# Optimization experiments

Measured on AMD Instinct MI355X. Metric: run time of the kernel, lower is better.

## Reference

```python
import jax, jax.numpy as jnp
import numpy as np

D_MODEL = 1024
NUM_HEADS = 16
HEAD_DIM = D_MODEL // NUM_HEADS
B, S = 2, 2048


def setup_inputs() -> dict:
    key = jax.random.key(0)
    ks = jax.random.split(key, 8)
    scale = 1.0 / np.sqrt(D_MODEL)
    inp = {
        "query": jax.random.normal(ks[0], (B, S, D_MODEL), jnp.float32),
        "key": jax.random.normal(ks[1], (B, S, D_MODEL), jnp.float32),
        "value": jax.random.normal(ks[2], (B, S, D_MODEL), jnp.float32),
        # causal mask, broadcastable over batch and heads
        "mask": jnp.tril(jnp.ones((S, S), dtype=bool))[None, None, :, :],
        # torch nn.Linear weights: y = x @ W.T (+ b)
        "Wq": jax.random.normal(ks[3], (D_MODEL, D_MODEL), jnp.float32) * scale,
        "Wk": jax.random.normal(ks[4], (D_MODEL, D_MODEL), jnp.float32) * scale,
        "Wv": jax.random.normal(ks[5], (D_MODEL, D_MODEL), jnp.float32) * scale,
        "Wo": jax.random.normal(ks[6], (D_MODEL, D_MODEL), jnp.float32) * scale,
        "bo": jax.random.normal(ks[7], (D_MODEL,), jnp.float32) * scale,
    }
    return inp


def _split_heads(x):
    b, s, _ = x.shape
    return x.reshape(b, s, NUM_HEADS, HEAD_DIM).transpose(0, 2, 1, 3)  # [B,H,S,Dh]


def reference(query, key, value, mask, Wq, Wk, Wv, Wo, bo):
    q = _split_heads(query @ Wq.T)
    k = _split_heads(key @ Wk.T)
    v = _split_heads(value @ Wv.T)
    scores = jnp.einsum("bhqd,bhkd->bhqk", q, k) / jnp.sqrt(jnp.float32(HEAD_DIM))
    scores = jnp.where(mask, scores, jnp.float32(-jnp.inf))
    attn = jax.nn.softmax(scores, axis=-1)
    out = jnp.einsum("bhqk,bhkd->bhqd", attn, v)  # [B,H,S,Dh]
    out = out.transpose(0, 2, 1, 3).reshape(query.shape[0], q.shape[2], D_MODEL)
    return out @ Wo.T + bo
```

## Files before the change

### kernel.cpp

```cpp
#include <hip/hip_runtime.h>
#include <hip/hip_bf16.h>

#define DM   1024
#define NH   16
#define HD   64
#define SEQ  2048
#define BATCH 2
#define MTOT (BATCH*SEQ)

typedef unsigned short u16;
typedef __attribute__((ext_vector_type(8))) short bf16x8;
typedef __attribute__((ext_vector_type(4))) float f32x4;

#define SC2F 0.1803368801111464f

__device__ __forceinline__ float bf2f(u16 h) {
  union { unsigned int i; float f; } u; u.i = ((unsigned int)h) << 16; return u.f;
}
__device__ __forceinline__ u16 f2bf(float f) {
  union { float f; unsigned int i; } u; u.f = f;
  unsigned int r = u.i + 0x7fffu + ((u.i >> 16) & 1u);
  return (u16)(r >> 16);
}
__device__ __forceinline__ unsigned int pk2(float lo, float hi) {
  union { float f; unsigned int u; } a, b; a.f = lo; b.f = hi;
  return ((a.u + 0x8000u) >> 16) | ((b.u + 0x8000u) & 0xFFFF0000u);
}
__device__ __forceinline__ unsigned int cvtpk(float lo, float hi) {
  unsigned int r;
  asm("v_cvt_pk_bf16_f32 %0, %1, %2" : "=v"(r) : "v"(lo), "v"(hi));
  return r;
}

__device__ __forceinline__ uint4 load8_bf16(const void* base, size_t elemOff, bool isf32) {
  if (!isf32) return *(const uint4*)((const u16*)base + elemOff);
  const float* f = (const float*)base + elemOff;
  f32x4 a = *(const f32x4*)f;
  f32x4 b = *(const f32x4*)(f + 4);
  union { u16 h[8]; uint4 v; } r;
  r.h[0]=f2bf(a[0]); r.h[1]=f2bf(a[1]); r.h[2]=f2bf(a[2]); r.h[3]=f2bf(a[3]);
  r.h[4]=f2bf(b[0]); r.h[5]=f2bf(b[1]); r.h[6]=f2bf(b[2]); r.h[7]=f2bf(b[3]);
  return r.v;
}

__global__ __launch_bounds__(256) void prep(
    const void* __restrict__ q, const void* __restrict__ k, const void* __restrict__ v,
    const void* __restrict__ wq, const void* __restrict__ wk, const void* __restrict__ wv,
    const void* __restrict__ wo, const void* __restrict__ bo,
    u16* __restrict__ Xq, u16* __restrict__ Xk, u16* __restrict__ Xv,
    u16* __restrict__ Wqb, u16* __restrict__ Wkb, u16* __restrict__ Wvb, u16* __restrict__ Wob,
    float* __restrict__ biasf, int* __restrict__ flag_out)
{
  const int tid = threadIdx.x;
  __shared__ int cnts[4];
  {
    const u16* qs = (const u16*)q;
    int e0 = (qs[tid*2]   >> 7) & 0xFF;
    int e1 = (qs[tid*2+1] >> 7) & 0xFF;
    int c = ((e0 >= 0x6E && e0 <= 0x8F) ? 1 : 0) + ((e1 >= 0x6E && e1 <= 0x8F) ? 1 : 0);
    c += __shfl_xor(c, 1);  c += __shfl_xor(c, 2);  c += __shfl_xor(c, 4);
    c += __shfl_xor(c, 8);  c += __shfl_xor(c, 16); c += __shfl_xor(c, 32);
    if ((tid & 63) == 0) cnts[tid >> 6] = c;
  }
  __syncthreads();
  const bool isf32 = (cnts[0] + cnts[1] + cnts[2] + cnts[3]) < 400;

  const int z = blockIdx.z;
  if (z == 7) {
    if (blockIdx.x == 0) {
      if (tid == 0) *flag_out = isf32 ? 0 : 1;
      for (int i = tid; i < DM; i += 256)
        biasf[i] = isf32 ? ((const float*)bo)[i] : bf2f(((const u16*)bo)[i]);
    }
    return;
  }
  const void* src; u16* dst; size_t n;
  switch (z) {
    case 0: src=q;  dst=Xq;  n=(size_t)MTOT*DM; break;
    case 1: src=k;  dst=Xk;  n=(size_t)MTOT*DM; break;
    case 2: src=v;  dst=Xv;  n=(size_t)MTOT*DM; break;
    case 3: src=wq; dst=Wqb; n=(size_t)DM*DM;   break;
    case 4: src=wk; dst=Wkb; n=(size_t)DM*DM;   break;
    case 5: src=wv; dst=Wvb; n=(size_t)DM*DM;   break;
    default: src=wo; dst=Wob; n=(size_t)DM*DM;  break;
  }
  const size_t stride = (size_t)gridDim.x * 256 * 8;
  for (size_t i = ((size_t)blockIdx.x * 256 + tid) * 8; i < n; i += stride)
    *(uint4*)(dst + i) = load8_bf16(src, i, isf32);
}

__device__ __forceinline__ void gld16(const u16* g, u16* l) {
  __builtin_amdgcn_global_load_lds(
      (const __attribute__((address_space(1))) void*)g,
      (__attribute__((address_space(3))) void*)l, 16, 0, 0);
}

__global__ __launch_bounds__(256) void gemm_qkv(
    const u16* __restrict__ X0, const u16* __restrict__ X1, const u16* __restrict__ X2,
    const u16* __restrict__ W0, const u16* __restrict__ W1, const u16* __restrict__ W2,
    u16* __restrict__ F0, u16* __restrict__ F1, u16* __restrict__ F2)
{
  __shared__ __align__(16) u16 smem[16384];
  u16* const A0 = smem;
  u16* const A1 = smem + 4096;
  u16* const B0 = smem + 8192;
  u16* const B1 = smem + 12288;

  const int zz = blockIdx.z;
  const u16* X = (zz==0) ? X0 : ((zz==1) ? X1 : X2);
  const u16* W = (zz==0) ? W0 : ((zz==1) ? W1 : W2);
  u16* outF    = (zz==0) ? F0 : ((zz==1) ? F1 : F2);

  const int tid = threadIdx.x;
  const int wave = tid >> 6, lane = tid & 63, quad = lane >> 4, l16 = lane & 15;
  const int wr = wave >> 1, wc = wave & 1;
  const int m0 = blockIdx.x * 128, n0 = blockIdx.y * 128;

  const int sg = ((lane & 3) ^ ((lane >> 3) & 3)) * 8;
  const int rS = wave*32 + (lane >> 2);
  const u16* gA0 = X + (size_t)(m0 + rS)*DM + sg;
  const u16* gA1 = X + (size_t)(m0 + rS + 16)*DM + sg;
  const u16* gB0 = W + (size_t)(n0 + rS)*DM + sg;
  const u16* gB1 = W + (size_t)(n0 + rS + 16)*DM + sg;
  const int so = wave*1024;

  const int xslot8 = (quad ^ ((l16 >> 1) & 3)) * 8;

  f32x4 acc[4][4];
#pragma unroll
  for (int i = 0; i < 4; i++)
#pragma unroll
    for (int j = 0; j < 4; j++) { acc[i][j][0]=0.f; acc[i][j][1]=0.f; acc[i][j][2]=0.f; acc[i][j][3]=0.f; }

  gld16(gA0, A0 + so);
  gld16(gA1, A0 + so + 512);
  gld16(gB0, B0 + so);
  gld16(gB1, B0 + so + 512);
  asm volatile("" ::: "memory");

  for (int k0 = 0; k0 < DM; k0 += 32) {
    const int cb = (k0 >> 5) & 1;
    u16* const Ab = cb ? A1 : A0;
    u16* const Bb = cb ? B1 : B0;
    if (k0 + 32 < DM) {
      u16* const An = cb ? A0 : A1;
      u16* const Bn = cb ? B0 : B1;
      gld16(gA0 + k0 + 32, An + so);
      gld16(gA1 + k0 + 32, An + so + 512);
      gld16(gB0 + k0 + 32, Bn + so);
      gld16(gB1 + k0 + 32, Bn + so + 512);
      asm volatile("s_waitcnt vmcnt(4)" ::: "memory");
    } else {
      asm volatile("s_waitcnt vmcnt(0)" ::: "memory");
    }
    __builtin_amdgcn_s_barrier();
    asm volatile("" ::: "memory");

    bf16x8 af[4], bfr[4];
#pragma unroll
    for (int fr = 0; fr < 4; fr++)
      af[fr] = *(const bf16x8*)&Ab[(wr*64 + fr*16 + l16)*32 + xslot8];
#pragma unroll
    for (int fc = 0; fc < 4; fc++)
      bfr[fc] = *(const bf16x8*)&Bb[(wc*64 + fc*16 + l16)*32 + xslot8];
#pragma unroll
    for (int fr = 0; fr < 4; fr++)
#pragma unroll
      for (int fc = 0; fc < 4; fc++)
        acc[fr][fc] = __builtin_amdgcn_mfma_f32_16x16x32_bf16(af[fr], bfr[fc], acc[fr][fc], 0, 0, 0);

    asm volatile("" ::: "memory");
    __builtin_amdgcn_s_barrier();
    asm volatile("" ::: "memory");
  }

  if (zz == 2) {
    u16* const Ts = smem;
    const int bb = m0 >> 11;
    const int s0 = m0 & (SEQ-1);
#pragma unroll
    for (int p = 0; p < 2; p++) {
      __syncthreads();
      if (wc == p) {
#pragma unroll
        for (int fr = 0; fr < 4; fr++) {
#pragma unroll
          for (int fc = 0; fc < 4; fc++) {
            const int dl = fc*16 + l16;
            const int sb = wr*64 + fr*16 + quad*4;
            const int slot = (sb >> 3) ^ (dl & 15);
            u16* rowp = &Ts[dl*128 + slot*8 + (sb & 7)];
            *(unsigned int*)(rowp)     = pk2(acc[fr][fc][0], acc[fr][fc][1]);
            *(unsigned int*)(rowp + 2) = pk2(acc[fr][fc][2], acc[fr][fc][3]);
          }
        }
      }
      __syncthreads();
      const int dl2 = tid >> 2, ch4 = tid & 3;
      const int hh = (n0 + p*64) >> 6;
      u16* dst = outF + ((size_t)(bb*NH + hh)*HD + dl2)*SEQ + s0 + ch4*32;
#pragma unroll
      for (int j = 0; j < 4; j++) {
        const int c  = ch4*4 + j;
        const int lo = (c >> 2)*32 + (c & 3)*4;
        const int hi = lo + 16;
        uint2 lo2 = *(const uint2*)&Ts[dl2*128 + (((lo >> 3) ^ (dl2 & 15))*8) + (lo & 7)];
        uint2 hi2 = *(const uint2*)&Ts[dl2*128 + (((hi >> 3) ^ (dl2 & 15))*8) + (hi & 7)];
        uint4 o; o.x = lo2.x; o.y = lo2.y; o.z = hi2.x; o.w = hi2.y;
        *(uint4*)&dst[j*8] = o;
      }
    }
    return;
  }

#pragma unroll
  for (int fr = 0; fr < 4; fr++) {
#pragma unroll
    for (int rr = 0; rr < 4; rr++) {
      const int m = m0 + wr*64 + fr*16 + quad*4 + rr;
#pragma unroll
      for (int fc = 0; fc < 4; fc++) {
        const int n = n0 + wc*64 + fc*16 + l16;
        float vv = acc[fr][fc][rr];
        if (zz == 0) vv *= SC2F;
        const int b = m >> 11, s = m & (SEQ-1), h = n >> 6, d = n & (HD-1);
        outF[((size_t)(b*NH + h)*SEQ + s)*HD + d] = f2bf(vv);
      }
    }
  }
}

__global__ __launch_bounds__(256) void gemm_out(
    const u16* __restrict__ X, const u16* __restrict__ W,
    const float* __restrict__ biasf, void* __restrict__ outP,
    const int* __restrict__ dflag)
{
  __shared__ __align__(16) u16 smem[12288];
  u16* const A0 = smem;
  u16* const A1 = smem + 4096;
  u16* const B0 = smem + 8192;
  u16* const B1 = smem + 10240;

  const int tid = threadIdx.x;
  const int wave = tid >> 6, lane = tid & 63, quad = lane >> 4, l16 = lane & 15;
  const int wr = wave >> 1, wc = wave & 1;
  const int m0 = blockIdx.x * 128, n0 = blockIdx.y * 64;

  const int sg = ((lane & 3) ^ ((lane >> 3) & 3)) * 8;
  const int rA = wave*32 + (lane >> 2);
  const int rB = wave*16 + (lane >> 2);
  const u16* gA0 = X + (size_t)(m0 + rA)*DM + sg;
  const u16* gA1 = X + (size_t)(m0 + rA + 16)*DM + sg;
  const u16* gB0 = W + (size_t)(n0 + rB)*DM + sg;
  const int soA = wave*1024, soB = wave*512;

  const int xslot8 = (quad ^ ((l16 >> 1) & 3)) * 8;

  f32x4 acc[4][2];
#pragma unroll
  for (int i = 0; i < 4; i++)
#pragma unroll
    for (int j = 0; j < 2; j++) { acc[i][j][0]=0.f; acc[i][j][1]=0.f; acc[i][j][2]=0.f; acc[i][j][3]=0.f; }

  gld16(gA0, A0 + soA);
  gld16(gA1, A0 + soA + 512);
  gld16(gB0, B0 + soB);
  asm volatile("" ::: "memory");

  for (int k0 = 0; k0 < DM; k0 += 32) {
    const int cb = (k0 >> 5) & 1;
    u16* const Ab = cb ? A1 : A0;
    u16* const Bb = cb ? B1 : B0;
    if (k0 + 32 < DM) {
      u16* const An = cb ? A0 : A1;
      u16* const Bn = cb ? B0 : B1;
      gld16(gA0 + k0 + 32, An + soA);
      gld16(gA1 + k0 + 32, An + soA + 512);
      gld16(gB0 + k0 + 32, Bn + soB);
      asm volatile("s_waitcnt vmcnt(3)" ::: "memory");
    } else {
      asm volatile("s_waitcnt vmcnt(0)" ::: "memory");
    }
    __builtin_amdgcn_s_barrier();
    asm volatile("" ::: "memory");

    bf16x8 af[4], bfr[2];
#pragma unroll
    for (int fr = 0; fr < 4; fr++)
      af[fr] = *(const bf16x8*)&Ab[(wr*64 + fr*16 + l16)*32 + xslot8];
#pragma unroll
    for (int fc = 0; fc < 2; fc++)
      bfr[fc] = *(const bf16x8*)&Bb[(wc*32 + fc*16 + l16)*32 + xslot8];
#pragma unroll
    for (int fr = 0; fr < 4; fr++)
#pragma unroll
      for (int fc = 0; fc < 2; fc++)
        acc[fr][fc] = __builtin_amdgcn_mfma_f32_16x16x32_bf16(af[fr], bfr[fc], acc[fr][fc], 0, 0, 0);

    asm volatile("" ::: "memory");
    __builtin_amdgcn_s_barrier();
    asm volatile("" ::: "memory");
  }

  const bool isf32 = (*dflag == 0);
#pragma unroll
  for (int fr = 0; fr < 4; fr++) {
#pragma unroll
    for (int rr = 0; rr < 4; rr++) {
      const int m = m0 + wr*64 + fr*16 + quad*4 + rr;
#pragma unroll
      for (int fc = 0; fc < 2; fc++) {
        const int n = n0 + wc*32 + fc*16 + l16;
        float vv = acc[fr][fc][rr] + biasf[n];
        if (isf32) ((float*)outP)[(size_t)m*DM + n] = vv;
        else       ((u16*)outP)[(size_t)m*DM + n]   = f2bf(vv);
      }
    }
  }
}

__global__ __launch_bounds__(256) void attn_mfma(
    const u16* __restrict__ Qb, const u16* __restrict__ Kb,
    const u16* __restrict__ Vtb,
    u16* __restrict__ Opart, float* __restrict__ mlpart)
{
  __shared__ u16 Ks[2][64*64];
  __shared__ u16 Vs[2][64*64];

  const int bh = blockIdx.x;
  const int pr = blockIdx.y, z = blockIdx.z;
  const u16* Qp = Qb  + (size_t)bh * SEQ * HD;
  const u16* Kp = Kb  + (size_t)bh * SEQ * HD;
  const u16* Vp = Vtb + (size_t)bh * HD * SEQ;

  const int tid  = threadIdx.x;
  const int wave = tid >> 6, lane = tid & 63, quad = lane >> 4, l16 = lane & 15;

  const int i0 = wave*128 + lane, i1 = i0 + 64;
  const int r0 = i0 >> 3, c0 = (i0 & 7) ^ (r0 & 7);
  const int r1 = i1 >> 3, c1 = (i1 & 7) ^ (r1 & 7);
  const int kq_off0 = r0*HD + c0*8;
  const int kq_off1 = r1*HD + c1*8;
  const int v_off0  = r0*SEQ + c0*8;
  const int v_off1  = r1*SEQ + c1*8;

  const int l7 = l16 & 7;
  const int ql = wave*16 + l16;
  const int so = wave*1024;

  for (int ph = 0; ph < 2; ph++) {
    const int qt = ph ? (31 - pr) : pr;
    const int n = qt + 1, half = (n + 1) >> 1;
    const int klo = z ? half : 0, khi = z ? n : half;
    const int q0 = qt * 64;
    const int qg = q0 + ql;

    const u16* qrow = Qp + (size_t)qg * HD;
    const bf16x8 bq0 = *(const bf16x8*)(qrow + quad*8);
    const bf16x8 bq1 = *(const bf16x8*)(qrow + 32 + quad*8);

    f32x4 O[4];
#pragma unroll
    for (int u = 0; u < 4; u++) { O[u][0]=0.f; O[u][1]=0.f; O[u][2]=0.f; O[u][3]=0.f; }
    float mi = -__builtin_inff(), li = 0.f;

    if (klo < khi) {
      gld16(Kp + klo*(64*HD) + kq_off0, &Ks[0][so]);
      gld16(Kp + klo*(64*HD) + kq_off1, &Ks[0][so + 512]);
      gld16(Vp + klo*64 + v_off0, &Vs[0][so]);
      gld16(Vp + klo*64 + v_off1, &Vs[0][so + 512]);
    }
    asm volatile("" ::: "memory");

    for (int kt = klo; kt < khi; kt++) {
      const int cb = (kt - klo) & 1;
      const u16* kb = &Ks[cb][0];
      const u16* vb = &Vs[cb][0];
      if (kt + 1 < khi) {
        u16* kn = &Ks[cb ^ 1][so];
        u16* vn = &Vs[cb ^ 1][so];
        gld16(Kp + (kt+1)*(64*HD) + kq_off0, kn);
        gld16(Kp + (kt+1)*(64*HD) + kq_off1, kn + 512);
        gld16(Vp + (kt+1)*64 + v_off0, vn);
        gld16(Vp + (kt+1)*64 + v_off1, vn + 512);
        asm volatile("s_waitcnt vmcnt(4)" ::: "memory");
      } else {
        asm volatile("s_waitcnt vmcnt(0)" ::: "memory");
      }
      __builtin_amdgcn_s_barrier();
      asm volatile("" ::: "memory");

      f32x4 st[4];
#pragma unroll
      for (int t = 0; t < 4; t++) { st[t][0]=0.f; st[t][1]=0.f; st[t][2]=0.f; st[t][3]=0.f; }
#pragma unroll
      for (int s = 0; s < 2; s++) {
        const bf16x8 bq = s ? bq1 : bq0;
        const int ch = s*4 + quad;
#pragma unroll
        for (int t = 0; t < 4; t++) {
          bf16x8 ak = *(const bf16x8*)&kb[((t*16 + l16)*8 + (ch ^ l7))*8];
          st[t] = __builtin_amdgcn_mfma_f32_16x16x32_bf16(ak, bq, st[t], 0, 0, 0);
        }
      }

      if (kt == qt) {
#pragma unroll
        for (int t = 0; t < 4; t++)
#pragma unroll
          for (int r = 0; r < 4; r++)
            if (kt*64 + t*16 + quad*4 + r > qg) st[t][r] = -__builtin_inff();
      }

      float a0 = fmaxf(fmaxf(st[0][0], st[0][1]), fmaxf(st[0][2], st[0][3]));
      float a1 = fmaxf(fmaxf(st[1][0], st[1][1]), fmaxf(st[1][2], st[1][3]));
      float a2 = fmaxf(fmaxf(st[2][0], st[2][1]), fmaxf(st[2][2], st[2][3]));
      float a3 = fmaxf(fmaxf(st[3][0], st[3][1]), fmaxf(st[3][2], st[3][3]));
      float mx = fmaxf(fmaxf(a0, a1), fmaxf(a2, a3));
      mx = fmaxf(mx, __shfl_xor(mx, 16));
      mx = fmaxf(mx, __shfl_xor(mx, 32));
      const float nm = fmaxf(mi, mx);
      const float al = exp2f(mi - nm);
      unsigned int w[4][2];
      float ps = 0.f;
#pragma unroll
      for (int t = 0; t < 4; t++) {
        float p0 = exp2f(st[t][0] - nm), p1 = exp2f(st[t][1] - nm);
        float p2 = exp2f(st[t][2] - nm), p3 = exp2f(st[t][3] - nm);
        ps += (p0 + p1) + (p2 + p3);
        w[t][0] = cvtpk(p0, p1);
        w[t][1] = cvtpk(p2, p3);
      }
      li = li * al + ps;
      mi = nm;
#pragma unroll
      for (int u = 0; u < 4; u++) {
        O[u][0] *= al; O[u][1] *= al; O[u][2] *= al; O[u][3] *= al;
      }

#pragma unroll
      for (int s = 0; s < 2; s++) {
        union { unsigned int u[4]; bf16x8 v; } bp;
        bp.u[0] = w[2*s][0];   bp.u[1] = w[2*s][1];
        bp.u[2] = w[2*s+1][0]; bp.u[3] = w[2*s+1][1];
        const int ch = s*4 + quad;
#pragma unroll
        for (int u = 0; u < 4; u++) {
          bf16x8 av = *(const bf16x8*)&vb[((u*16 + l16)*8 + (ch ^ l7))*8];
          O[u] = __builtin_amdgcn_mfma_f32_16x16x32_bf16(av, bp.v, O[u], 0, 0, 0);
        }
      }

      asm volatile("" ::: "memory");
      __builtin_amdgcn_s_barrier();
      asm volatile("" ::: "memory");
    }

    li += __shfl_xor(li, 16);
    li += __shfl_xor(li, 32);

    const int pi = (bh*32 + qt)*2 + z;
    u16* op = Opart + (size_t)pi*4096 + ql*64;
#pragma unroll
    for (int u = 0; u < 4; u++) {
      uint2 u2; u2.x = pk2(O[u][0], O[u][1]); u2.y = pk2(O[u][2], O[u][3]);
      *(uint2*)&op[u*16 + quad*4] = u2;
    }
    if (quad == 0) {
      float2 ml2; ml2.x = mi; ml2.y = li;
      *(float2*)&mlpart[(size_t)pi*128 + ql*2] = ml2;
    }
  }
}

__global__ __launch_bounds__(64) void attn_merge(
    const u16* __restrict__ Opart, const float* __restrict__ mlpart,
    u16* __restrict__ aO)
{
  const int g = blockIdx.x;
  const int bh = g & 31, qt = g >> 5;
  const int b = bh >> 4, h = bh & 15;
  const int t = threadIdx.x;
  const int pi0 = (bh*32 + qt)*2, pi1 = pi0 + 1;

  const float2 ml0 = *(const float2*)&mlpart[(size_t)pi0*128 + t*2];
  const float2 ml1 = *(const float2*)&mlpart[(size_t)pi1*128 + t*2];
  const float M = fmaxf(ml0.x, ml1.x);
  float w0 = exp2f(ml0.x - M), w1 = exp2f(ml1.x - M);
  const float inv = 1.0f / (w0*ml0.y + w1*ml1.y);
  w0 *= inv; w1 *= inv;

  const u16* o0 = Opart + (size_t)pi0*4096 + t*64;
  const u16* o1 = Opart + (size_t)pi1*4096 + t*64;
  u16* out = aO + (size_t)(b*SEQ + qt*64 + t)*DM + h*HD;
#pragma unroll
  for (int d0 = 0; d0 < 64; d0 += 8) {
    union { uint4 v; u16 h[8]; } a, c; union { uint4 v; u16 h[8]; } bb;
    a.v  = *(const uint4*)&o0[d0];
    bb.v = *(const uint4*)&o1[d0];
#pragma unroll
    for (int j = 0; j < 8; j += 2) {
      float x0 = w0*bf2f(a.h[j])   + w1*bf2f(bb.h[j]);
      float x1 = w0*bf2f(a.h[j+1]) + w1*bf2f(bb.h[j+1]);
      unsigned int pk = pk2(x0, x1);
      c.h[j] = (u16)(pk & 0xFFFF); c.h[j+1] = (u16)(pk >> 16);
    }
    *(uint4*)&out[d0] = c.v;
  }
}

extern "C" void kernel_launch(void* const* d_in, const int* in_sizes, int n_in,
                              void* d_out, int out_size, void* d_ws, size_t ws_size,
                              hipStream_t stream) {
  const void* q  = d_in[0];
  const void* k  = d_in[1];
  const void* v  = d_in[2];
  const void* wq = d_in[4];
  const void* wk = d_in[5];
  const void* wv = d_in[6];
  const void* wo = d_in[7];
  const void* bo = d_in[8];

  const size_t TX = (size_t)MTOT*DM;
  const size_t TW = (size_t)DM*DM;
  u16* ws  = (u16*)d_ws;
  u16* Xq  = ws;
  u16* Xk  = ws + TX;
  u16* Xv  = ws + 2*TX;
  u16* Wqb = ws + 3*TX;
  u16* Wkb = Wqb + TW;
  u16* Wvb = Wqb + 2*TW;
  u16* Wob = Wqb + 3*TW;
  u16* Qw  = ws + 3*TX + 4*TW;
  u16* Kw  = Qw + TX;
  u16* Vt  = Qw + 2*TX;
  u16*   Opart  = Xk;
  float* mlpart = (float*)Wqb;
  u16*   aO     = Xq;
  float* biasf  = (float*)(Qw + 3*TX);
  int*   fl     = (int*)(biasf + DM);

  dim3 blk(256);
  prep<<<dim3(512, 1, 8), blk, 0, stream>>>(q, k, v, wq, wk, wv, wo, bo,
      Xq, Xk, Xv, Wqb, Wkb, Wvb, Wob, biasf, fl);
  gemm_qkv<<<dim3(MTOT/128, DM/128, 3), blk, 0, stream>>>(
      Xq, Xk, Xv, Wqb, Wkb, Wvb, Qw, Kw, Vt);
  attn_mfma<<<dim3(BATCH*NH, 16, 2), blk, 0, stream>>>(Qw, Kw, Vt, Opart, mlpart);
  attn_merge<<<dim3(32*32), dim3(64), 0, stream>>>(Opart, mlpart, aO);
  gemm_out<<<dim3(MTOT/128, DM/64), blk, 0, stream>>>(aO, Wob, biasf, d_out, fl);
}
```

Baseline: 231.5 us.

## Pair adjacent query tiles per block to share K/V tiles; add lazy softmax rescale

Each attention block now processes two consecutive 64-row query tiles against the same streamed K/V tiles. This halves the K/V loads and LDS traffic per query row, and the y-dimension of the grid is halved to match. The online softmax now rescales only when some lane's row max grows by more than 8 (in log2 units), and the row sums are kept as per-lane vectors. The trade-off is more registers per thread and half as many blocks, which lowers occupancy and parallelism. The lazy rescale lets unnormalized probabilities grow up to 2^8 before they are converted to bf16.

```diff
diff --git a/kernel.cpp b/kernel.cpp
--- a/kernel.cpp
+++ b/kernel.cpp
@@ -328,7 +328,7 @@
   __shared__ u16 Vs[2][64*64];
 
   const int bh = blockIdx.x;
-  const int pr = blockIdx.y, z = blockIdx.z;
+  const int py = blockIdx.y, z = blockIdx.z;
   const u16* Qp = Qb  + (size_t)bh * SEQ * HD;
   const u16* Kp = Kb  + (size_t)bh * SEQ * HD;
   const u16* Vp = Vtb + (size_t)bh * HD * SEQ;
@@ -349,20 +349,29 @@
   const int so = wave*1024;
 
   for (int ph = 0; ph < 2; ph++) {
-    const int qt = ph ? (31 - pr) : pr;
-    const int n = qt + 1, half = (n + 1) >> 1;
-    const int klo = z ? half : 0, khi = z ? n : half;
-    const int q0 = qt * 64;
-    const int qg = q0 + ql;
-
-    const u16* qrow = Qp + (size_t)qg * HD;
-    const bf16x8 bq0 = *(const bf16x8*)(qrow + quad*8);
-    const bf16x8 bq1 = *(const bf16x8*)(qrow + 32 + quad*8);
-
-    f32x4 O[4];
-#pragma unroll
-    for (int u = 0; u < 4; u++) { O[u][0]=0.f; O[u][1]=0.f; O[u][2]=0.f; O[u][3]=0.f; }
-    float mi = -__builtin_inff(), li = 0.f;
+    const int P = ph ? (15 - py) : py;
+    const int qtA = 2*P, qtB = 2*P + 1;
+    const int nB = qtB + 1;
+    const int half = P + 1;
+    const int klo = z ? half : 0, khi = z ? nB : half;
+    const int qgA = qtA*64 + ql;
+    const int qgB = qgA + 64;
+
+    const u16* qrowA = Qp + (size_t)qgA * HD;
+    const u16* qrowB = Qp + (size_t)qgB * HD;
+    const bf16x8 bqA0 = *(const bf16x8*)(qrowA + quad*8);
+    const bf16x8 bqA1 = *(const bf16x8*)(qrowA + 32 + quad*8);
+    const bf16x8 bqB0 = *(const bf16x8*)(qrowB + quad*8);
+    const bf16x8 bqB1 = *(const bf16x8*)(qrowB + 32 + quad*8);
+
+    f32x4 OA[4], OB[4];
+#pragma unroll
+    for (int u = 0; u < 4; u++) {
+      OA[u][0]=0.f; OA[u][1]=0.f; OA[u][2]=0.f; OA[u][3]=0.f;
+      OB[u][0]=0.f; OB[u][1]=0.f; OB[u][2]=0.f; OB[u][3]=0.f;
+    }
+    float miA = -3.0e38f, miB = -3.0e38f;
+    f32x4 lvA = {0.f,0.f,0.f,0.f}, lvB = {0.f,0.f,0.f,0.f};
 
     if (klo < khi) {
       gld16(Kp + klo*(64*HD) + kq_off0, &Ks[0][so]);
@@ -390,64 +399,107 @@
       __builtin_amdgcn_s_barrier();
       asm volatile("" ::: "memory");
 
-      f32x4 st[4];
-#pragma unroll
-      for (int t = 0; t < 4; t++) { st[t][0]=0.f; st[t][1]=0.f; st[t][2]=0.f; st[t][3]=0.f; }
+      f32x4 stA[4], stB[4];
+#pragma unroll
+      for (int t = 0; t < 4; t++) {
+        stA[t][0]=0.f; stA[t][1]=0.f; stA[t][2]=0.f; stA[t][3]=0.f;
+        stB[t][0]=0.f; stB[t][1]=0.f; stB[t][2]=0.f; stB[t][3]=0.f;
+      }
 #pragma unroll
       for (int s = 0; s < 2; s++) {
-        const bf16x8 bq = s ? bq1 : bq0;
+        const bf16x8 bqA = s ? bqA1 : bqA0;
+        const bf16x8 bqB = s ? bqB1 : bqB0;
         const int ch = s*4 + quad;
 #pragma unroll
         for (int t = 0; t < 4; t++) {
           bf16x8 ak = *(const bf16x8*)&kb[((t*16 + l16)*8 + (ch ^ l7))*8];
-          st[t] = __builtin_amdgcn_mfma_f32_16x16x32_bf16(ak, bq, st[t], 0, 0, 0);
+          stA[t] = __builtin_amdgcn_mfma_f32_16x16x32_bf16(ak, bqA, stA[t], 0, 0, 0);
+          stB[t] = __builtin_amdgcn_mfma_f32_16x16x32_bf16(ak, bqB, stB[t], 0, 0, 0);
         }
       }
 
-      if (kt == qt) {
+      if (kt >= qtA) {
 #pragma unroll
         for (int t = 0; t < 4; t++)
 #pragma unroll
           for (int r = 0; r < 4; r++)
-            if (kt*64 + t*16 + quad*4 + r > qg) st[t][r] = -__builtin_inff();
-      }
-
-      float a0 = fmaxf(fmaxf(st[0][0], st[0][1]), fmaxf(st[0][2], st[0][3]));
-      float a1 = fmaxf(fmaxf(st[1][0], st[1][1]), fmaxf(st[1][2], st[1][3]));
-      float a2 = fmaxf(fmaxf(st[2][0], st[2][1]), fmaxf(st[2][2], st[2][3]));
-      float a3 = fmaxf(fmaxf(st[3][0], st[3][1]), fmaxf(st[3][2], st[3][3]));
-      float mx = fmaxf(fmaxf(a0, a1), fmaxf(a2, a3));
-      mx = fmaxf(mx, __shfl_xor(mx, 16));
-      mx = fmaxf(mx, __shfl_xor(mx, 32));
-      const float nm = fmaxf(mi, mx);
-      const float al = exp2f(mi - nm);
-      unsigned int w[4][2];
-      float ps = 0.f;
-#pragma unroll
-      for (int t = 0; t < 4; t++) {
-        float p0 = exp2f(st[t][0] - nm), p1 = exp2f(st[t][1] - nm);
-        float p2 = exp2f(st[t][2] - nm), p3 = exp2f(st[t][3] - nm);
-        ps += (p0 + p1) + (p2 + p3);
-        w[t][0] = cvtpk(p0, p1);
-        w[t][1] = cvtpk(p2, p3);
-      }
-      li = li * al + ps;
-      mi = nm;
-#pragma unroll
-      for (int u = 0; u < 4; u++) {
-        O[u][0] *= al; O[u][1] *= al; O[u][2] *= al; O[u][3] *= al;
+            if (kt*64 + t*16 + quad*4 + r > qgA) stA[t][r] = -__builtin_inff();
+      }
+      if (kt == qtB) {
+#pragma unroll
+        for (int t = 0; t < 4; t++)
+#pragma unroll
+          for (int r = 0; r < 4; r++)
+            if (kt*64 + t*16 + quad*4 + r > qgB) stB[t][r] = -__builtin_inff();
+      }
+
+      f32x4 ma = __builtin_elementwise_max(
+          __builtin_elementwise_max(stA[0], stA[1]),
+          __builtin_elementwise_max(stA[2], stA[3]));
+      f32x4 mb = __builtin_elementwise_max(
+          __builtin_elementwise_max(stB[0], stB[1]),
+          __builtin_elementwise_max(stB[2], stB[3]));
+      float mxA = fmaxf(fmaxf(ma[0], ma[1]), fmaxf(ma[2], ma[3]));
+      float mxB = fmaxf(fmaxf(mb[0], mb[1]), fmaxf(mb[2], mb[3]));
+      mxA = fmaxf(mxA, __shfl_xor(mxA, 16));
+      mxA = fmaxf(mxA, __shfl_xor(mxA, 32));
+      mxB = fmaxf(mxB, __shfl_xor(mxB, 16));
+      mxB = fmaxf(mxB, __shfl_xor(mxB, 32));
+
+      if (__any((mxA > miA + 8.0f) || (mxB > miB + 8.0f))) {
+        const float nmA = fmaxf(miA, mxA);
+        const float nmB = fmaxf(miB, mxB);
+        const float alA = exp2f(miA - nmA);
+        const float alB = exp2f(miB - nmB);
+        miA = nmA; miB = nmB;
+        const f32x4 avA = {alA, alA, alA, alA};
+        const f32x4 avB = {alB, alB, alB, alB};
+        lvA *= avA; lvB *= avB;
+        OA[0] *= avA; OA[1] *= avA; OA[2] *= avA; OA[3] *= avA;
+        OB[0] *= avB; OB[1] *= avB; OB[2] *= avB; OB[3] *= avB;
+      }
+
+      unsigned int wA[4][2], wB[4][2];
+      {
+        const f32x4 mv = {miA, miA, miA, miA};
+        f32x4 e0 = stA[0] - mv, e1 = stA[1] - mv, e2 = stA[2] - mv, e3 = stA[3] - mv;
+        e0[0]=exp2f(e0[0]); e0[1]=exp2f(e0[1]); e0[2]=exp2f(e0[2]); e0[3]=exp2f(e0[3]);
+        e1[0]=exp2f(e1[0]); e1[1]=exp2f(e1[1]); e1[2]=exp2f(e1[2]); e1[3]=exp2f(e1[3]);
+        e2[0]=exp2f(e2[0]); e2[1]=exp2f(e2[1]); e2[2]=exp2f(e2[2]); e2[3]=exp2f(e2[3]);
+        e3[0]=exp2f(e3[0]); e3[1]=exp2f(e3[1]); e3[2]=exp2f(e3[2]); e3[3]=exp2f(e3[3]);
+        wA[0][0]=cvtpk(e0[0],e0[1]); wA[0][1]=cvtpk(e0[2],e0[3]);
+        wA[1][0]=cvtpk(e1[0],e1[1]); wA[1][1]=cvtpk(e1[2],e1[3]);
+        wA[2][0]=cvtpk(e2[0],e2[1]); wA[2][1]=cvtpk(e2[2],e2[3]);
+        wA[3][0]=cvtpk(e3[0],e3[1]); wA[3][1]=cvtpk(e3[2],e3[3]);
+        lvA += (e0 + e1) + (e2 + e3);
+      }
+      {
+        const f32x4 mv = {miB, miB, miB, miB};
+        f32x4 e0 = stB[0] - mv, e1 = stB[1] - mv, e2 = stB[2] - mv, e3 = stB[3] - mv;
+        e0[0]=exp2f(e0[0]); e0[1]=exp2f(e0[1]); e0[2]=exp2f(e0[2]); e0[3]=exp2f(e0[3]);
+        e1[0]=exp2f(e1[0]); e1[1]=exp2f(e1[1]); e1[2]=exp2f(e1[2]); e1[3]=exp2f(e1[3]);
+        e2[0]=exp2f(e2[0]); e2[1]=exp2f(e2[1]); e2[2]=exp2f(e2[2]); e2[3]=exp2f(e2[3]);
+        e3[0]=exp2f(e3[0]); e3[1]=exp2f(e3[1]); e3[2]=exp2f(e3[2]); e3[3]=exp2f(e3[3]);
+        wB[0][0]=cvtpk(e0[0],e0[1]); wB[0][1]=cvtpk(e0[2],e0[3]);
+        wB[1][0]=cvtpk(e1[0],e1[1]); wB[1][1]=cvtpk(e1[2],e1[3]);
+        wB[2][0]=cvtpk(e2[0],e2[1]); wB[2][1]=cvtpk(e2[2],e2[3]);
+        wB[3][0]=cvtpk(e3[0],e3[1]); wB[3][1]=cvtpk(e3[2],e3[3]);
+        lvB += (e0 + e1) + (e2 + e3);
       }
 
 #pragma unroll
       for (int s = 0; s < 2; s++) {
-        union { unsigned int u[4]; bf16x8 v; } bp;
-        bp.u[0] = w[2*s][0];   bp.u[1] = w[2*s][1];
-        bp.u[2] = w[2*s+1][0]; bp.u[3] = w[2*s+1][1];
+        union { unsigned int u[4]; bf16x8 v; } bpA, bpB;
+        bpA.u[0] = wA[2*s][0];   bpA.u[1] = wA[2*s][1];
+        bpA.u[2] = wA[2*s+1][0]; bpA.u[3] = wA[2*s+1][1];
+        bpB.u[0] = wB[2*s][0];   bpB.u[1] = wB[2*s][1];
+        bpB.u[2] = wB[2*s+1][0]; bpB.u[3] = wB[2*s+1][1];
         const int ch = s*4 + quad;
 #pragma unroll
         for (int u = 0; u < 4; u++) {
           bf16x8 av = *(const bf16x8*)&vb[((u*16 + l16)*8 + (ch ^ l7))*8];
-          O[u] = __builtin_amdgcn_mfma_f32_16x16x32_bf16(av, bp.v, O[u], 0, 0, 0);
+          OA[u] = __builtin_amdgcn_mfma_f32_16x16x32_bf16(av, bpA.v, OA[u], 0, 0, 0);
+          OB[u] = __builtin_amdgcn_mfma_f32_16x16x32_bf16(av, bpB.v, OB[u], 0, 0, 0);
         }
       }
 
@@ -456,19 +508,29 @@
       asm volatile("" ::: "memory");
     }
 
-    li += __shfl_xor(li, 16);
-    li += __shfl_xor(li, 32);
-
-    const int pi = (bh*32 + qt)*2 + z;
-    u16* op = Opart + (size_t)pi*4096 + ql*64;
+    float lsA = (lvA[0] + lvA[1]) + (lvA[2] + lvA[3]);
+    lsA += __shfl_xor(lsA, 16);
+    lsA += __shfl_xor(lsA, 32);
+    float lsB = (lvB[0] + lvB[1]) + (lvB[2] + lvB[3]);
+    lsB += __shfl_xor(lsB, 16);
+    lsB += __shfl_xor(lsB, 32);
+
+    const int piA = (bh*32 + qtA)*2 + z;
+    const int piB = (bh*32 + qtB)*2 + z;
+    u16* opA = Opart + (size_t)piA*4096 + ql*64;
+    u16* opB = Opart + (size_t)piB*4096 + ql*64;
 #pragma unroll
     for (int u = 0; u < 4; u++) {
-      uint2 u2; u2.x = pk2(O[u][0], O[u][1]); u2.y = pk2(O[u][2], O[u][3]);
-      *(uint2*)&op[u*16 + quad*4] = u2;
+      uint2 a2; a2.x = pk2(OA[u][0], OA[u][1]); a2.y = pk2(OA[u][2], OA[u][3]);
+      *(uint2*)&opA[u*16 + quad*4] = a2;
+      uint2 b2; b2.x = pk2(OB[u][0], OB[u][1]); b2.y = pk2(OB[u][2], OB[u][3]);
+      *(uint2*)&opB[u*16 + quad*4] = b2;
     }
     if (quad == 0) {
-      float2 ml2; ml2.x = mi; ml2.y = li;
-      *(float2*)&mlpart[(size_t)pi*128 + ql*2] = ml2;
+      float2 mA; mA.x = miA; mA.y = lsA;
+      *(float2*)&mlpart[(size_t)piA*128 + ql*2] = mA;
+      float2 mB; mB.x = miB; mB.y = lsB;
+      *(float2*)&mlpart[(size_t)piB*128 + ql*2] = mB;
     }
   }
 }
@@ -545,7 +607,7 @@
       Xq, Xk, Xv, Wqb, Wkb, Wvb, Wob, biasf, fl);
   gemm_qkv<<<dim3(MTOT/128, DM/128, 3), blk, 0, stream>>>(
       Xq, Xk, Xv, Wqb, Wkb, Wvb, Qw, Kw, Vt);
-  attn_mfma<<<dim3(BATCH*NH, 16, 2), blk, 0, stream>>>(Qw, Kw, Vt, Opart, mlpart);
+  attn_mfma<<<dim3(BATCH*NH, 8, 2), blk, 0, stream>>>(Qw, Kw, Vt, Opart, mlpart);
   attn_merge<<<dim3(32*32), dim3(64), 0, stream>>>(Opart, mlpart, aO);
   gemm_out<<<dim3(MTOT/128, DM/64), blk, 0, stream>>>(aO, Wob, biasf, d_out, fl);
 }
```

After: 235.4 us. About the same (+1.7%).
